# Kernel tuning notes

Measured on AMD Instinct MI355X. Metric: run time of the kernel, lower is better.

## Reference

```python
import jax, jax.numpy as jnp
import numpy as np

SEQ_LEN = 200
BATCH = 32768
H = 4  # LSTM hidden size


def _lstm_layer(x, Wih, Whh, bih, bhh):
    """PyTorch-semantics LSTM layer. x: [B,T,D] -> [B,T,H]. Gate order i,f,g,o."""
    # precompute input contribution for all timesteps: [B,T,4H]
    xg = jnp.einsum('btd,gd->btg', x, Wih) + bih + bhh

    def step(carry, xt):
        h, c = carry
        g = xt + h @ Whh.T  # [B,4H]
        i, f, gg, o = jnp.split(g, 4, axis=-1)
        c = jax.nn.sigmoid(f) * c + jax.nn.sigmoid(i) * jnp.tanh(gg)
        h = jax.nn.sigmoid(o) * jnp.tanh(c)
        return (h, c), h

    B = x.shape[0]
    z = jnp.zeros((B, Whh.shape[1]), x.dtype)
    _, hs = jax.lax.scan(step, (z, z), jnp.swapaxes(xg, 0, 1))  # [T,B,H]
    return jnp.swapaxes(hs, 0, 1)


def _lstm2(x, Wih0, Whh0, bih0, bhh0, Wih1, Whh1, bih1, bhh1):
    h = _lstm_layer(x, Wih0, Whh0, bih0, bhh0)
    return _lstm_layer(h, Wih1, Whh1, bih1, bhh1)


def setup_inputs() -> dict:
    key = jax.random.key(0)
    ks = iter(jax.random.split(key, 64))
    def p(shape, s=0.1):
        return jax.random.normal(next(ks), shape, jnp.float32) * s
    d = {"x": jax.random.normal(next(ks), (BATCH, 2, SEQ_LEN), jnp.float32)}
    for r in ("r0", "r1"):
        d[f"{r}_Wih0"] = p((4 * H, 1)); d[f"{r}_Whh0"] = p((4 * H, H))
        d[f"{r}_bih0"] = p((4 * H,));  d[f"{r}_bhh0"] = p((4 * H,))
        d[f"{r}_Wih1"] = p((4 * H, H)); d[f"{r}_Whh1"] = p((4 * H, H))
        d[f"{r}_bih1"] = p((4 * H,));  d[f"{r}_bhh1"] = p((4 * H,))
    d["Wp"] = p((40, 2 * SEQ_LEN)); d["bp"] = p((40,))
    d["WH"] = p((128, 4 * SEQ_LEN)); d["bH"] = p((128,))
    d["WL"] = p((128, 4 * SEQ_LEN)); d["bL"] = p((128,))
    d["W1"] = p((80, 256)); d["b1"] = p((80,))
    d["W2"] = p((40, 80)); d["b2"] = p((40,))
    d["W3"] = p((1, 80)); d["b3"] = p((1,))
    return d


def reference(x,
              r0_Wih0, r0_Whh0, r0_bih0, r0_bhh0, r0_Wih1, r0_Whh1, r0_bih1, r0_bhh1,
              r1_Wih0, r1_Whh0, r1_bih0, r1_bhh0, r1_Wih1, r1_Whh1, r1_bih1, r1_bhh1,
              Wp, bp, WH, bH, WL, bL, W1, b1, W2, b2, W3, b3):
    B = x.shape[0]
    x_flat = x.reshape(B, 2 * SEQ_LEN)
    other = x_flat @ Wp.T + bp  # [B,40]

    Hx = x[:, 0, :, None]  # [B,T,1]
    Lx = x[:, 1, :, None]
    Hh = _lstm2(Hx, r0_Wih0, r0_Whh0, r0_bih0, r0_bhh0, r0_Wih1, r0_Whh1, r0_bih1, r0_bhh1)
    Lh = _lstm2(Lx, r1_Wih0, r1_Whh0, r1_bih0, r1_bhh0, r1_Wih1, r1_Whh1, r1_bih1, r1_bhh1)
    Hf = jnp.tanh(Hh.reshape(B, 4 * SEQ_LEN) @ WH.T + bH)  # [B,128]
    Lf = jnp.tanh(Lh.reshape(B, 4 * SEQ_LEN) @ WL.T + bL)
    z = jnp.concatenate([Hf, Lf], axis=1)  # [B,256]
    z = jnp.tanh(z @ W1.T + b1)  # [B,80]
    z = jnp.tanh(z @ W2.T + b2)  # [B,40]
    z = jnp.concatenate([z, other], axis=1)  # [B,80]
    return jax.nn.sigmoid(z @ W3.T + b3)  # [B,1]
```

## Files before the change

kernel.cpp:

```cpp
#include <hip/hip_runtime.h>
#include <hip/hip_bf16.h>

#define BATCH 32768
#define TSEQ 200

typedef __attribute__((ext_vector_type(8))) short short8;
typedef __attribute__((ext_vector_type(4))) float floatx4;
typedef __attribute__((ext_vector_type(2))) float f32x2;

#if __has_builtin(__builtin_amdgcn_exp2f)
__device__ __forceinline__ float EXP2(float x) { return __builtin_amdgcn_exp2f(x); }
#else
__device__ __forceinline__ float EXP2(float x) {
    float r; asm("v_exp_f32 %0, %1" : "=v"(r) : "v"(x)); return r;
}
#endif
__device__ __forceinline__ float RCP(float x) { return __builtin_amdgcn_rcpf(x); }

__device__ __forceinline__ float fast_sigmoid(float x) {
    return RCP(1.0f + EXP2(-1.4426950408889634f * x));
}
__device__ __forceinline__ float fast_tanh(float x) {
    float e = EXP2(2.8853900817779268f * x);
    return 1.0f - 2.0f * RCP(e + 1.0f);
}
__device__ __forceinline__ short f2bfs(float v) {
    __hip_bfloat16 h = __float2bfloat16(v);
    return __builtin_bit_cast(short, h);
}
__device__ __forceinline__ f32x2 splat2(float x) { f32x2 v; v[0] = x; v[1] = x; return v; }
__device__ __forceinline__ f32x2 pkfma(f32x2 a, f32x2 b, f32x2 c) {
    return __builtin_elementwise_fma(a, b, c);
}
__device__ __forceinline__ void keepv(f32x2& v) {
    float a = v[0], b = v[1];
    asm volatile("" : "+v"(a), "+v"(b));
    v[0] = a; v[1] = b;
}
template <int K>
__device__ __forceinline__ float qb(float v) {
    int i = __builtin_bit_cast(int, v);
    int r = __builtin_amdgcn_update_dpp(i, i, K * 0x55, 0xf, 0xf, false);
    return __builtin_bit_cast(float, r);
}
__device__ __forceinline__ void async16(void* lds, const void* g) {
    __builtin_amdgcn_global_load_lds(
        (const __attribute__((address_space(1))) unsigned int*)g,
        (__attribute__((address_space(3))) unsigned int*)lds, 16, 0, 0);
}

#define S_SIG (-1.4426950408889634f)
#define S_TANH (2.8853900817779268f)

#define WS_HH  0
#define WS_WHB 104857600
#define WS_WLB (WS_WHB + 204800)
#define WS_W1B (WS_WLB + 204800)
#define WS_W2B (WS_W1B + 40960)
#define WS_U   (WS_W2B + 9216)

struct LW { const float* p[16]; };

__global__ __launch_bounds__(256) void k_prep(
    const float* __restrict__ WH, const float* __restrict__ WL,
    const float* __restrict__ W1, const float* __restrict__ W2,
    const float* __restrict__ W3, const float* __restrict__ Wp,
    const float* __restrict__ bp, const float* __restrict__ b3,
    __hip_bfloat16* __restrict__ WHbf, __hip_bfloat16* __restrict__ WLbf,
    __hip_bfloat16* __restrict__ W1bf, __hip_bfloat16* __restrict__ W2bf,
    float* __restrict__ u)
{
    int gid = blockIdx.x * 256 + threadIdx.x;
    int n = gid / 800, k = gid - n * 800;
    int t = k >> 2, q = k & 3;
    int kp = (t >> 2) * 16 + q * 4 + (t & 3);
    int dst = n * 800 + kp;
    WHbf[dst] = __float2bfloat16(WH[gid]);
    WLbf[dst] = __float2bfloat16(WL[gid]);
    if (gid < 20480) W1bf[gid] = __float2bfloat16(W1[gid]);
    if (gid < 4608) {
        int rr = gid / 96, cc = gid - rr * 96;
        float v = (rr < 40 && cc < 80) ? W2[rr * 80 + cc] : 0.0f;
        W2bf[gid] = __float2bfloat16(v);
    }
    if (gid < 400) {
        float a = 0.f;
        for (int j = 0; j < 40; ++j) a = fmaf(W3[40 + j], Wp[j * 400 + gid], a);
        u[gid] = a;
    } else if (gid == 400) {
        float a = b3[0];
        for (int j = 0; j < 40; ++j) a = fmaf(W3[40 + j], bp[j], a);
        u[400] = a;
    }
}

__global__ __launch_bounds__(256)
__attribute__((amdgpu_waves_per_eu(4, 4))) void k_fused(
    const float* __restrict__ x, LW w, const float* __restrict__ u,
    __hip_bfloat16* __restrict__ hh,
    const __hip_bfloat16* __restrict__ WHbf, const __hip_bfloat16* __restrict__ WLbf,
    const float* __restrict__ bH, const float* __restrict__ bL,
    const __hip_bfloat16* __restrict__ W1bf, const __hip_bfloat16* __restrict__ W2bf,
    const float* __restrict__ b1, const float* __restrict__ b2,
    const float* __restrict__ W3, float* __restrict__ out)
{
    __shared__ __align__(16) char smem[33024];
    short* Bse = (short*)smem;
    short* zl  = (short*)smem;
    short* z1l = (short*)(smem + 17024);
    float* z2l = (float*)(smem + 23808);
    float* ot  = (float*)(smem + 32768);

    int tid = threadIdx.x;
    int q = tid & 3;
    int g = tid >> 2;
    int r = tid >> 7;
    int b = blockIdx.x * 32 + (g & 31);

    const float* Wih0 = w.p[r * 8 + 0];
    const float* Whh0 = w.p[r * 8 + 1];
    const float* bih0 = w.p[r * 8 + 2];
    const float* bhh0 = w.p[r * 8 + 3];
    const float* Wih1 = w.p[r * 8 + 4];
    const float* Whh1 = w.p[r * 8 + 5];
    const float* bih1 = w.p[r * 8 + 6];
    const float* bhh1 = w.p[r * 8 + 7];

    f32x2 wx0p[2], bb0p[2], bb1p[2], whh0p[2][4], wih1p[2][4], whh1p[2][4];
#pragma unroll
    for (int p = 0; p < 2; ++p) {
#pragma unroll
        for (int c = 0; c < 2; ++c) {
            int G = 2 * p + c;
            int j = 4 * G + q;
            float sc = (G == 2) ? S_TANH : S_SIG;
            wx0p[p][c] = Wih0[j] * sc;
            bb0p[p][c] = (bih0[j] + bhh0[j]) * sc;
            bb1p[p][c] = (bih1[j] + bhh1[j]) * sc;
#pragma unroll
            for (int k = 0; k < 4; ++k) {
                whh0p[p][k][c] = Whh0[j * 4 + k] * sc;
                wih1p[p][k][c] = Wih1[j * 4 + k] * sc;
                whh1p[p][k][c] = Whh1[j * 4 + k] * sc;
            }
        }
    }
#pragma unroll
    for (int p = 0; p < 2; ++p) {
        keepv(wx0p[p]); keepv(bb0p[p]); keepv(bb1p[p]);
#pragma unroll
        for (int k = 0; k < 4; ++k) {
            keepv(whh0p[p][k]); keepv(wih1p[p][k]); keepv(whh1p[p][k]);
        }
    }

    const float* xp = x + ((size_t)b * 2 + r) * TSEQ;
    const float* up = u + r * TSEQ;
    __hip_bfloat16* hp = hh + ((size_t)r * BATCH + b) * 800 + q * 4;

    float h0 = 0.f, c0 = 0.f, h1 = 0.f, c1 = 0.f, accO = 0.f;

    for (int tb = 0; tb < TSEQ; tb += 4) {
        float4 xv = *(const float4*)(xp + tb);
        float4 uv = *(const float4*)(up + tb);
        float xa[4] = {xv.x, xv.y, xv.z, xv.w};
        float ua[4] = {uv.x, uv.y, uv.z, uv.w};
        float hb[4];
#pragma unroll
        for (int j = 0; j < 4; ++j) {
            float xt = xa[j];
            accO = fmaf(xt, ua[j], accO);

            float a0 = qb<0>(h0), a1 = qb<1>(h0), a2 = qb<2>(h0), a3 = qb<3>(h0);
            f32x2 g0 = pkfma(splat2(xt), wx0p[0], bb0p[0]);
            f32x2 g1 = pkfma(splat2(xt), wx0p[1], bb0p[1]);
            g0 = pkfma(whh0p[0][0], splat2(a0), g0); g1 = pkfma(whh0p[1][0], splat2(a0), g1);
            g0 = pkfma(whh0p[0][1], splat2(a1), g0); g1 = pkfma(whh0p[1][1], splat2(a1), g1);
            g0 = pkfma(whh0p[0][2], splat2(a2), g0); g1 = pkfma(whh0p[1][2], splat2(a2), g1);
            g0 = pkfma(whh0p[0][3], splat2(a3), g0); g1 = pkfma(whh0p[1][3], splat2(a3), g1);
            float ig = RCP(1.0f + EXP2(g0[0]));
            float fg = RCP(1.0f + EXP2(g0[1]));
            float og = RCP(1.0f + EXP2(g1[1]));
            float tg = 1.0f - 2.0f * RCP(EXP2(g1[0]) + 1.0f);
            c0 = fmaf(fg, c0, ig * tg);
            float th0 = 1.0f - 2.0f * RCP(EXP2(S_TANH * c0) + 1.0f);
            h0 = og * th0;

            float p0 = qb<0>(h0), p1 = qb<1>(h0), p2 = qb<2>(h0), p3 = qb<3>(h0);
            float q0 = qb<0>(h1), q1 = qb<1>(h1), q2 = qb<2>(h1), q3 = qb<3>(h1);
            g0 = bb1p[0]; g1 = bb1p[1];
            g0 = pkfma(wih1p[0][0], splat2(p0), g0); g1 = pkfma(wih1p[1][0], splat2(p0), g1);
            g0 = pkfma(wih1p[0][1], splat2(p1), g0); g1 = pkfma(wih1p[1][1], splat2(p1), g1);
            g0 = pkfma(wih1p[0][2], splat2(p2), g0); g1 = pkfma(wih1p[1][2], splat2(p2), g1);
            g0 = pkfma(wih1p[0][3], splat2(p3), g0); g1 = pkfma(wih1p[1][3], splat2(p3), g1);
            g0 = pkfma(whh1p[0][0], splat2(q0), g0); g1 = pkfma(whh1p[1][0], splat2(q0), g1);
            g0 = pkfma(whh1p[0][1], splat2(q1), g0); g1 = pkfma(whh1p[1][1], splat2(q1), g1);
            g0 = pkfma(whh1p[0][2], splat2(q2), g0); g1 = pkfma(whh1p[1][2], splat2(q2), g1);
            g0 = pkfma(whh1p[0][3], splat2(q3), g0); g1 = pkfma(whh1p[1][3], splat2(q3), g1);
            ig = RCP(1.0f + EXP2(g0[0]));
            fg = RCP(1.0f + EXP2(g0[1]));
            og = RCP(1.0f + EXP2(g1[1]));
            tg = 1.0f - 2.0f * RCP(EXP2(g1[0]) + 1.0f);
            c1 = fmaf(fg, c1, ig * tg);
            float th1 = 1.0f - 2.0f * RCP(EXP2(S_TANH * c1) + 1.0f);
            h1 = og * th1;
            hb[j] = h1;
        }
        ushort4 pk;
        pk.x = (unsigned short)f2bfs(hb[0]);
        pk.y = (unsigned short)f2bfs(hb[1]);
        pk.z = (unsigned short)f2bfs(hb[2]);
        pk.w = (unsigned short)f2bfs(hb[3]);
        *(ushort4*)(hp + tb * 4) = pk;
    }
    if (q == 0) ot[g] = accO;
    __syncthreads();

    int wv = tid >> 6, lane = tid & 63, l15 = lane & 15, quad = lane >> 4;
    int b0 = blockIdx.x * 32;
    int f = wv >> 1, mt = wv & 1;

    const __hip_bfloat16* gB0 = WHbf + (size_t)(wv * 16 + (tid & 15)) * 800 + ((tid >> 4) & 3) * 8;
    const __hip_bfloat16* gB2 = WLbf + (size_t)(wv * 16 + (tid & 15)) * 800 + ((tid >> 4) & 3) * 8;
    const __hip_bfloat16* Ab =
        hh + ((size_t)f * BATCH + b0 + mt * 16 + l15) * 800 + quad * 8;

#define PF(kc, buf)                                                    \
    do {                                                               \
        char* lb_ = smem + (buf) * 16384 + wv * 1024;                  \
        async16(lb_,          gB0 + (kc) * 32);                        \
        async16(lb_ + 4096,   gB0 + 64 * 800 + (kc) * 32);             \
        async16(lb_ + 8192,   gB2 + (kc) * 32);                        \
        async16(lb_ + 12288,  gB2 + 64 * 800 + (kc) * 32);             \
    } while (0)

    floatx4 acc[8] = {};
    short8 af = *(const short8*)(const void*)Ab;
    PF(0, 0);
    for (int kc = 0; kc < 25; ++kc) {
        __syncthreads();
        short8 afn = af;
        if (kc < 24) {
            PF(kc + 1, (kc + 1) & 1);
            afn = *(const short8*)(const void*)(Ab + (kc + 1) * 32);
        }
        const short* Bb = Bse + (kc & 1) * 8192 + f * 4096 + lane * 8;
#pragma unroll
        for (int nt = 0; nt < 8; ++nt) {
            short8 bfr = *(const short8*)(const void*)(Bb + nt * 512);
            acc[nt] = __builtin_amdgcn_mfma_f32_16x16x32_bf16(af, bfr, acc[nt], 0, 0, 0);
        }
        af = afn;
    }
#undef PF
    __syncthreads();

    {
        const float* bias = f ? bL : bH;
#pragma unroll
        for (int nt = 0; nt < 8; ++nt) {
            float bb = bias[nt * 16 + l15];
            int c = f * 128 + nt * 16 + l15;
#pragma unroll
            for (int rg = 0; rg < 4; ++rg) {
                int m = mt * 16 + quad * 4 + rg;
                zl[m * 264 + c] = f2bfs(fast_tanh(acc[nt][rg] + bb));
            }
        }
    }
    __syncthreads();

    if (wv < 2) {
        floatx4 a1[5] = {};
        for (int kc = 0; kc < 8; ++kc) {
            short8 afz = *(const short8*)(const void*)
                &zl[(wv * 16 + l15) * 264 + kc * 32 + quad * 8];
#pragma unroll
            for (int nt = 0; nt < 5; ++nt) {
                short8 bfr = *(const short8*)(const void*)
                    (W1bf + (size_t)(nt * 16 + l15) * 256 + kc * 32 + quad * 8);
                a1[nt] = __builtin_amdgcn_mfma_f32_16x16x32_bf16(afz, bfr, a1[nt], 0, 0, 0);
            }
        }
#pragma unroll
        for (int nt = 0; nt < 5; ++nt) {
            int n = nt * 16 + l15;
            float bb = b1[n];
#pragma unroll
            for (int rg = 0; rg < 4; ++rg)
                z1l[(wv * 16 + quad * 4 + rg) * 104 + n] = f2bfs(fast_tanh(a1[nt][rg] + bb));
        }
    } else {
        int i0 = tid - 128;
        for (int i = i0; i < 512; i += 128) {
            int rr = i >> 4, cc = 80 + (i & 15);
            z1l[rr * 104 + cc] = 0;
        }
    }
    __syncthreads();

    if (wv < 2) {
        floatx4 a2[3] = {};
        for (int kc = 0; kc < 3; ++kc) {
            short8 afz = *(const short8*)(const void*)
                &z1l[(wv * 16 + l15) * 104 + kc * 32 + quad * 8];
#pragma unroll
            for (int nt = 0; nt < 3; ++nt) {
                short8 bfr = *(const short8*)(const void*)
                    (W2bf + (size_t)(nt * 16 + l15) * 96 + kc * 32 + quad * 8);
                a2[nt] = __builtin_amdgcn_mfma_f32_16x16x32_bf16(afz, bfr, a2[nt], 0, 0, 0);
            }
        }
#pragma unroll
        for (int nt = 0; nt < 3; ++nt) {
            int n = nt * 16 + l15;
            if (n < 40) {
                float bb = b2[n];
#pragma unroll
                for (int rg = 0; rg < 4; ++rg)
                    z2l[(wv * 16 + quad * 4 + rg) * 44 + n] = fast_tanh(a2[nt][rg] + bb);
            }
        }
    }
    __syncthreads();

    if (tid < 32) {
        float s = u[400] + ot[tid] + ot[32 + tid];
        for (int j = 0; j < 40; ++j) s = fmaf(z2l[tid * 44 + j], W3[j], s);
        out[b0 + tid] = fast_sigmoid(s);
    }
}

extern "C" void kernel_launch(void* const* d_in, const int* in_sizes, int n_in,
                              void* d_out, int out_size, void* d_ws, size_t ws_size,
                              hipStream_t stream)
{
    const float* x = (const float*)d_in[0];
    LW w;
    for (int i = 0; i < 16; ++i) w.p[i] = (const float*)d_in[1 + i];
    const float* Wp = (const float*)d_in[17];
    const float* bp = (const float*)d_in[18];
    const float* WH = (const float*)d_in[19];
    const float* bH = (const float*)d_in[20];
    const float* WL = (const float*)d_in[21];
    const float* bL = (const float*)d_in[22];
    const float* W1 = (const float*)d_in[23];
    const float* b1 = (const float*)d_in[24];
    const float* W2 = (const float*)d_in[25];
    const float* b2 = (const float*)d_in[26];
    const float* W3 = (const float*)d_in[27];
    const float* b3 = (const float*)d_in[28];

    char* ws = (char*)d_ws;
    __hip_bfloat16* hh   = (__hip_bfloat16*)(ws + WS_HH);
    __hip_bfloat16* WHbf = (__hip_bfloat16*)(ws + WS_WHB);
    __hip_bfloat16* WLbf = (__hip_bfloat16*)(ws + WS_WLB);
    __hip_bfloat16* W1bf = (__hip_bfloat16*)(ws + WS_W1B);
    __hip_bfloat16* W2bf = (__hip_bfloat16*)(ws + WS_W2B);
    float* u = (float*)(ws + WS_U);
    float* out = (float*)d_out;

    k_prep<<<400, 256, 0, stream>>>(WH, WL, W1, W2, W3, Wp, bp, b3,
                                    WHbf, WLbf, W1bf, W2bf, u);
    k_fused<<<1024, 256, 0, stream>>>(x, w, u, hh, WHbf, WLbf, bH, bL,
                                      W1bf, W2bf, b1, b2, W3, out);
}
```

Baseline: 318.0 us.

## Skew two LSTM layers so layer1 step t and layer0 step t+1 run concurrently

Restructures the recurrent loop as a wavefront: each round computes layer 1 at time t and layer 0 at time t+1 from the same broadcast h0, so the two gate chains become independent and can interleave. This shortens the serial dependency chain per timestep and removes one set of DPP broadcasts. It adds a prologue and epilogue for the skew and removes the asm register-pinning of weights, which may change register allocation.

```diff
diff --git a/kernel.cpp b/kernel.cpp
--- a/kernel.cpp
+++ b/kernel.cpp
@@ -31,11 +31,6 @@
 __device__ __forceinline__ f32x2 splat2(float x) { f32x2 v; v[0] = x; v[1] = x; return v; }
 __device__ __forceinline__ f32x2 pkfma(f32x2 a, f32x2 b, f32x2 c) {
     return __builtin_elementwise_fma(a, b, c);
-}
-__device__ __forceinline__ void keepv(f32x2& v) {
-    float a = v[0], b = v[1];
-    asm volatile("" : "+v"(a), "+v"(b));
-    v[0] = a; v[1] = b;
 }
 template <int K>
 __device__ __forceinline__ float qb(float v) {
@@ -94,6 +89,54 @@
     }
 }
 
+template <int M>
+__device__ __forceinline__ float lstm_round(
+    float xt, float& h0, float& c0, float& h1, float& c1,
+    const f32x2 (&wx0p)[2], const f32x2 (&bb0p)[2], const f32x2 (&whh0p)[2][4],
+    const f32x2 (&bb1p)[2], const f32x2 (&wih1p)[2][4], const f32x2 (&whh1p)[2][4])
+{
+    float a0 = qb<0>(h0), a1 = qb<1>(h0), a2 = qb<2>(h0), a3 = qb<3>(h0);
+    float h1out = 0.f;
+
+    if (M != 1) {
+        float q0 = qb<0>(h1), q1 = qb<1>(h1), q2 = qb<2>(h1), q3 = qb<3>(h1);
+        f32x2 G0 = bb1p[0], G1 = bb1p[1];
+        G0 = pkfma(wih1p[0][0], splat2(a0), G0); G1 = pkfma(wih1p[1][0], splat2(a0), G1);
+        G0 = pkfma(wih1p[0][1], splat2(a1), G0); G1 = pkfma(wih1p[1][1], splat2(a1), G1);
+        G0 = pkfma(wih1p[0][2], splat2(a2), G0); G1 = pkfma(wih1p[1][2], splat2(a2), G1);
+        G0 = pkfma(wih1p[0][3], splat2(a3), G0); G1 = pkfma(wih1p[1][3], splat2(a3), G1);
+        G0 = pkfma(whh1p[0][0], splat2(q0), G0); G1 = pkfma(whh1p[1][0], splat2(q0), G1);
+        G0 = pkfma(whh1p[0][1], splat2(q1), G0); G1 = pkfma(whh1p[1][1], splat2(q1), G1);
+        G0 = pkfma(whh1p[0][2], splat2(q2), G0); G1 = pkfma(whh1p[1][2], splat2(q2), G1);
+        G0 = pkfma(whh1p[0][3], splat2(q3), G0); G1 = pkfma(whh1p[1][3], splat2(q3), G1);
+        float ig = RCP(1.0f + EXP2(G0[0]));
+        float fg = RCP(1.0f + EXP2(G0[1]));
+        float og = RCP(1.0f + EXP2(G1[1]));
+        float tg = 1.0f - 2.0f * RCP(EXP2(G1[0]) + 1.0f);
+        c1 = fmaf(fg, c1, ig * tg);
+        float th1 = 1.0f - 2.0f * RCP(EXP2(S_TANH * c1) + 1.0f);
+        h1 = og * th1;
+        h1out = h1;
+    }
+
+    if (M != 2) {
+        f32x2 g0 = pkfma(splat2(xt), wx0p[0], bb0p[0]);
+        f32x2 g1 = pkfma(splat2(xt), wx0p[1], bb0p[1]);
+        g0 = pkfma(whh0p[0][0], splat2(a0), g0); g1 = pkfma(whh0p[1][0], splat2(a0), g1);
+        g0 = pkfma(whh0p[0][1], splat2(a1), g0); g1 = pkfma(whh0p[1][1], splat2(a1), g1);
+        g0 = pkfma(whh0p[0][2], splat2(a2), g0); g1 = pkfma(whh0p[1][2], splat2(a2), g1);
+        g0 = pkfma(whh0p[0][3], splat2(a3), g0); g1 = pkfma(whh0p[1][3], splat2(a3), g1);
+        float ig = RCP(1.0f + EXP2(g0[0]));
+        float fg = RCP(1.0f + EXP2(g0[1]));
+        float og = RCP(1.0f + EXP2(g1[1]));
+        float tg = 1.0f - 2.0f * RCP(EXP2(g1[0]) + 1.0f);
+        c0 = fmaf(fg, c0, ig * tg);
+        float th0 = 1.0f - 2.0f * RCP(EXP2(S_TANH * c0) + 1.0f);
+        h0 = og * th0;
+    }
+    return h1out;
+}
+
 __global__ __launch_bounds__(256)
 __attribute__((amdgpu_waves_per_eu(4, 4))) void k_fused(
     const float* __restrict__ x, LW w, const float* __restrict__ u,
@@ -145,14 +188,6 @@
             }
         }
     }
-#pragma unroll
-    for (int p = 0; p < 2; ++p) {
-        keepv(wx0p[p]); keepv(bb0p[p]); keepv(bb1p[p]);
-#pragma unroll
-        for (int k = 0; k < 4; ++k) {
-            keepv(whh0p[p][k]); keepv(wih1p[p][k]); keepv(whh1p[p][k]);
-        }
-    }
 
     const float* xp = x + ((size_t)b * 2 + r) * TSEQ;
     const float* up = u + r * TSEQ;
@@ -160,51 +195,24 @@
 
     float h0 = 0.f, c0 = 0.f, h1 = 0.f, c1 = 0.f, accO = 0.f;
 
-    for (int tb = 0; tb < TSEQ; tb += 4) {
-        float4 xv = *(const float4*)(xp + tb);
-        float4 uv = *(const float4*)(up + tb);
-        float xa[4] = {xv.x, xv.y, xv.z, xv.w};
-        float ua[4] = {uv.x, uv.y, uv.z, uv.w};
+    float4 xv_prev = *(const float4*)xp;
+    float4 uv_prev = *(const float4*)up;
+
+    accO = fmaf(xv_prev.x, uv_prev.x, accO);
+    lstm_round<1>(xv_prev.x, h0, c0, h1, c1,
+                  wx0p, bb0p, whh0p, bb1p, wih1p, whh1p);
+
+    for (int tb = 0; tb <= 192; tb += 4) {
+        float4 xv_new = *(const float4*)(xp + tb + 4);
+        float4 uv_new = *(const float4*)(up + tb + 4);
+        float xc[4] = {xv_prev.y, xv_prev.z, xv_prev.w, xv_new.x};
+        float uc[4] = {uv_prev.y, uv_prev.z, uv_prev.w, uv_new.x};
         float hb[4];
 #pragma unroll
         for (int j = 0; j < 4; ++j) {
-            float xt = xa[j];
-            accO = fmaf(xt, ua[j], accO);
-
-            float a0 = qb<0>(h0), a1 = qb<1>(h0), a2 = qb<2>(h0), a3 = qb<3>(h0);
-            f32x2 g0 = pkfma(splat2(xt), wx0p[0], bb0p[0]);
-            f32x2 g1 = pkfma(splat2(xt), wx0p[1], bb0p[1]);
-            g0 = pkfma(whh0p[0][0], splat2(a0), g0); g1 = pkfma(whh0p[1][0], splat2(a0), g1);
-            g0 = pkfma(whh0p[0][1], splat2(a1), g0); g1 = pkfma(whh0p[1][1], splat2(a1), g1);
-            g0 = pkfma(whh0p[0][2], splat2(a2), g0); g1 = pkfma(whh0p[1][2], splat2(a2), g1);
-            g0 = pkfma(whh0p[0][3], splat2(a3), g0); g1 = pkfma(whh0p[1][3], splat2(a3), g1);
-            float ig = RCP(1.0f + EXP2(g0[0]));
-            float fg = RCP(1.0f + EXP2(g0[1]));
-            float og = RCP(1.0f + EXP2(g1[1]));
-            float tg = 1.0f - 2.0f * RCP(EXP2(g1[0]) + 1.0f);
-            c0 = fmaf(fg, c0, ig * tg);
-            float th0 = 1.0f - 2.0f * RCP(EXP2(S_TANH * c0) + 1.0f);
-            h0 = og * th0;
-
-            float p0 = qb<0>(h0), p1 = qb<1>(h0), p2 = qb<2>(h0), p3 = qb<3>(h0);
-            float q0 = qb<0>(h1), q1 = qb<1>(h1), q2 = qb<2>(h1), q3 = qb<3>(h1);
-            g0 = bb1p[0]; g1 = bb1p[1];
-            g0 = pkfma(wih1p[0][0], splat2(p0), g0); g1 = pkfma(wih1p[1][0], splat2(p0), g1);
-            g0 = pkfma(wih1p[0][1], splat2(p1), g0); g1 = pkfma(wih1p[1][1], splat2(p1), g1);
-            g0 = pkfma(wih1p[0][2], splat2(p2), g0); g1 = pkfma(wih1p[1][2], splat2(p2), g1);
-            g0 = pkfma(wih1p[0][3], splat2(p3), g0); g1 = pkfma(wih1p[1][3], splat2(p3), g1);
-            g0 = pkfma(whh1p[0][0], splat2(q0), g0); g1 = pkfma(whh1p[1][0], splat2(q0), g1);
-            g0 = pkfma(whh1p[0][1], splat2(q1), g0); g1 = pkfma(whh1p[1][1], splat2(q1), g1);
-            g0 = pkfma(whh1p[0][2], splat2(q2), g0); g1 = pkfma(whh1p[1][2], splat2(q2), g1);
-            g0 = pkfma(whh1p[0][3], splat2(q3), g0); g1 = pkfma(whh1p[1][3], splat2(q3), g1);
-            ig = RCP(1.0f + EXP2(g0[0]));
-            fg = RCP(1.0f + EXP2(g0[1]));
-            og = RCP(1.0f + EXP2(g1[1]));
-            tg = 1.0f - 2.0f * RCP(EXP2(g1[0]) + 1.0f);
-            c1 = fmaf(fg, c1, ig * tg);
-            float th1 = 1.0f - 2.0f * RCP(EXP2(S_TANH * c1) + 1.0f);
-            h1 = og * th1;
-            hb[j] = h1;
+            accO = fmaf(xc[j], uc[j], accO);
+            hb[j] = lstm_round<0>(xc[j], h0, c0, h1, c1,
+                                  wx0p, bb0p, whh0p, bb1p, wih1p, whh1p);
         }
         ushort4 pk;
         pk.x = (unsigned short)f2bfs(hb[0]);
@@ -212,6 +220,27 @@
         pk.z = (unsigned short)f2bfs(hb[2]);
         pk.w = (unsigned short)f2bfs(hb[3]);
         *(ushort4*)(hp + tb * 4) = pk;
+        xv_prev = xv_new; uv_prev = uv_new;
+    }
+
+    {
+        float xc[3] = {xv_prev.y, xv_prev.z, xv_prev.w};
+        float uc[3] = {uv_prev.y, uv_prev.z, uv_prev.w};
+        float hb[4];
+#pragma unroll
+        for (int j = 0; j < 3; ++j) {
+            accO = fmaf(xc[j], uc[j], accO);
+            hb[j] = lstm_round<0>(xc[j], h0, c0, h1, c1,
+                                  wx0p, bb0p, whh0p, bb1p, wih1p, whh1p);
+        }
+        hb[3] = lstm_round<2>(0.f, h0, c0, h1, c1,
+                              wx0p, bb0p, whh0p, bb1p, wih1p, whh1p);
+        ushort4 pk;
+        pk.x = (unsigned short)f2bfs(hb[0]);
+        pk.y = (unsigned short)f2bfs(hb[1]);
+        pk.z = (unsigned short)f2bfs(hb[2]);
+        pk.w = (unsigned short)f2bfs(hb[3]);
+        *(ushort4*)(hp + 196 * 4) = pk;
     }
     if (q == 0) ot[g] = accO;
     __syncthreads();
```

Result: faster. 308.2 us (-3.1%).
